# Performance work log

Hardware: AMD Instinct MI355X
Metric: run time of the kernel (lower is better)

Reference implementation:

```python
import jax, jax.numpy as jnp
import numpy as np

QUERY_DIM = 3072
HEADS = 24
HEAD_DIM = 128
INNER = HEADS * HEAD_DIM  # 3072
MLP_HIDDEN = int(QUERY_DIM * 4.0)  # 12288
MLP_MULT = 2
EPS = 1e-5
B, S = 1, 4096


def setup_inputs() -> dict:
    key = jax.random.key(0)
    ks = jax.random.split(key, 8)
    hidden_states = jax.random.normal(ks[0], (B, S, QUERY_DIM), dtype=jnp.float32)
    # rotary angles for half the head dim (interleaved / non-neox style)
    t = jnp.arange(S, dtype=jnp.float32)[:, None]
    inv_freq = 1.0 / (10000.0 ** (jnp.arange(0, HEAD_DIM, 2, dtype=jnp.float32) / HEAD_DIM))
    ang = t * inv_freq[None, :]
    cos = jnp.cos(ang)
    sin = jnp.sin(ang)
    W_qkv_mlp = jax.random.normal(ks[1], (QUERY_DIM, 3 * INNER + MLP_HIDDEN * MLP_MULT), dtype=jnp.float32) * 0.02
    W_out = jax.random.normal(ks[2], (INNER + MLP_HIDDEN, QUERY_DIM), dtype=jnp.float32) * 0.02
    b_out = jnp.zeros((QUERY_DIM,), dtype=jnp.float32)
    norm_q_w = jnp.ones((HEAD_DIM,), dtype=jnp.float32)
    norm_k_w = jnp.ones((HEAD_DIM,), dtype=jnp.float32)
    return {"hidden_states": hidden_states, "cos": cos, "sin": sin,
            "W_qkv_mlp": W_qkv_mlp, "W_out": W_out, "b_out": b_out,
            "norm_q_w": norm_q_w, "norm_k_w": norm_k_w}


def _rmsnorm(x, w, eps=EPS):
    var = jnp.mean(jnp.square(x), axis=-1, keepdims=True)
    return x * jax.lax.rsqrt(var + eps) * w


def _rope_interleaved(x, cos, sin):
    # x: [B,S,H,D]; cos/sin: [S, D//2]. Non-neox: rotate interleaved pairs.
    x1 = x[..., 0::2]
    x2 = x[..., 1::2]
    c = cos[None, :, None, :]
    s = sin[None, :, None, :]
    o1 = x1 * c - x2 * s
    o2 = x2 * c + x1 * s
    return jnp.stack([o1, o2], axis=-1).reshape(x.shape)


def reference(hidden_states, cos, sin, W_qkv_mlp, W_out, b_out, norm_q_w, norm_k_w):
    h = hidden_states @ W_qkv_mlp  # [B,S, 3*INNER + 2*MLP_HIDDEN]
    qkv, mlp = jnp.split(h, [3 * INNER], axis=-1)
    q, k, v = jnp.split(qkv, 3, axis=-1)
    q = q.reshape(B, S, HEADS, HEAD_DIM)
    k = k.reshape(B, S, HEADS, HEAD_DIM)
    v = v.reshape(B, S, HEADS, HEAD_DIM)
    q = _rmsnorm(q, norm_q_w)
    k = _rmsnorm(k, norm_k_w)
    q = _rope_interleaved(q, cos, sin)
    k = _rope_interleaved(k, cos, sin)
    scale = 1.0 / np.sqrt(HEAD_DIM)
    scores = jnp.einsum('bqhd,bkhd->bhqk', q, k) * scale
    probs = jax.nn.softmax(scores, axis=-1)
    attn = jnp.einsum('bhqk,bkhd->bqhd', probs, v)
    attn = attn.reshape(B, S, INNER)
    m1, m2 = jnp.split(mlp, 2, axis=-1)
    mlp_out = jax.nn.silu(m1) * m2
    out = jnp.concatenate([attn, mlp_out], axis=-1) @ W_out + b_out
    return out
```

## Files before the change

### kernel.cpp

```cpp
#include <hip/hip_runtime.h>

typedef short shortx8 __attribute__((ext_vector_type(8)));
typedef short shortx4 __attribute__((ext_vector_type(4)));
typedef float floatx4 __attribute__((ext_vector_type(4)));
typedef float floatx16 __attribute__((ext_vector_type(16)));
typedef unsigned short u16;
typedef unsigned int u32;

#define GLB(x) ((const __attribute__((address_space(1))) void*)(x))
#define LDSC(x) ((__attribute__((address_space(3))) void*)(x))
#define BARRIER()                                  \
  do {                                             \
    __builtin_amdgcn_sched_barrier(0);             \
    __builtin_amdgcn_s_barrier();                  \
    __builtin_amdgcn_sched_barrier(0);             \
  } while (0)
#define WAITV6() asm volatile("s_waitcnt vmcnt(6)" ::: "memory")
#define WAITV8() asm volatile("s_waitcnt vmcnt(8)" ::: "memory")
#define WAITLGKM(N)                                          \
  do {                                                       \
    asm volatile("s_waitcnt lgkmcnt(" #N ")");               \
    __builtin_amdgcn_sched_barrier(0);                       \
  } while (0)

__device__ __forceinline__ float bf2f(u16 u) {
  unsigned x = ((unsigned)u) << 16;
  float f;
  __builtin_memcpy(&f, &x, 4);
  return f;
}
__device__ __forceinline__ u16 f2bf(float f) {
  unsigned x;
  __builtin_memcpy(&x, &f, 4);
  x += 0x7fffu + ((x >> 16) & 1u);
  return (u16)(x >> 16);
}
__device__ __forceinline__ u32 pk_bf16(float lo, float hi) {
  u32 r;
  asm("v_cvt_pk_bf16_f32 %0, %1, %2" : "=v"(r) : "v"(lo), "v"(hi));
  return r;
}

__global__ __launch_bounds__(256) void cast_bf16(const float* __restrict__ src,
                                                 u16* __restrict__ dst) {
  const size_t i = ((size_t)blockIdx.x * 256 + threadIdx.x) << 3;
  floatx4 a = *(const floatx4*)(src + i);
  floatx4 b = *(const floatx4*)(src + i + 4);
  shortx8 o;
#pragma unroll
  for (int e = 0; e < 4; ++e) {
    o[e] = (short)f2bf(a[e]);
    o[e + 4] = (short)f2bf(b[e]);
  }
  *(shortx8*)(dst + i) = o;
}

__global__ __launch_bounds__(256) void transpose_cast(const float* __restrict__ src,
                                                      u16* __restrict__ dst,
                                                      int R, int C, int perm) {
  __shared__ u16 T[64 * 72];
  const int tiles_c = C >> 6;
  const int r0 = (blockIdx.x / tiles_c) << 6;
  const int c0 = (blockIdx.x % tiles_c) << 6;
  const int tid = threadIdx.x;
  const int rl = tid >> 4;
  const int cb = (tid & 15) << 2;
#pragma unroll
  for (int rr = 0; rr < 4; ++rr) {
    const int row = rr * 16 + rl;
    floatx4 v = *(const floatx4*)(src + (size_t)(r0 + row) * C + c0 + cb);
#pragma unroll
    for (int i = 0; i < 4; ++i) T[(cb + i) * 72 + row] = f2bf(v[i]);
  }
  __syncthreads();
  int dbase = c0;
  if (perm && c0 >= 9216) {
    if (c0 < 21504) { const int u = c0 - 9216;  dbase = 9216 + ((u >> 7) << 8) + (u & 64); }
    else            { const int u = c0 - 21504; dbase = 9216 + ((u >> 7) << 8) + 128 + (u & 64); }
  }
#pragma unroll
  for (int ii = 0; ii < 2; ++ii) {
    const int chunk = tid + (ii << 8);
    const int cr = chunk >> 3;
    const int r8 = (chunk & 7) << 3;
    shortx8 v = *(const shortx8*)(T + cr * 72 + r8);
    *(shortx8*)(dst + (size_t)(dbase + cr) * R + r0 + r8) = v;
  }
}

template <int MODE>
__global__ __launch_bounds__(512, 2) void gemm8(const u16* __restrict__ A,
                                                const u16* __restrict__ B,
                                                void* __restrict__ Cout,
                                                u16* __restrict__ CC2,
                                                int M, int N, int K, int Ksub) {
  __shared__ u16 lds[8 * 8192];

  const int nbm = M >> 8;
  const int nwg = nbm * (N >> 8);
  const int cpx = nwg >> 3;
  const int wg = ((int)blockIdx.x & 7) * cpx + ((int)blockIdx.x >> 3);
  const int bm = wg % nbm;
  const int bn = wg / nbm;
  const int koff = (int)blockIdx.y * Ksub;

  const int tid = threadIdx.x;
  const int lane = tid & 63;
  const int w = tid >> 6;
  const int wm = w >> 2;
  const int wn = w & 3;
  const int l15 = lane & 15;
  const int l4 = lane >> 4;
  const int NT = Ksub >> 6;

  const int lrow = lane >> 2;
  const int lblk = lane & 3;

#define UNIT(buf, mat, ks) (lds + (((buf) * 4 + (mat) * 2 + (ks)) << 13))

  const u16* Abase = A + (size_t)bm * 256 * K + koff;
  const u16* Bbase = B + (size_t)bn * 256 * K + koff;

  auto STAGE = [&](int mat, int ks, int buf, int t) {
    const u16* gb = mat ? Bbase : Abase;
#pragma unroll
    for (int j = 0; j < 2; ++j) {
      const int row = (w * 2 + j) * 16 + lrow;
      const int sblk = lblk ^ ((row >> 1) & 3);
      const u16* src = gb + (size_t)row * K + (t << 6) + (ks << 5) + (sblk << 3);
      __builtin_amdgcn_global_load_lds(GLB(src),
                                       LDSC(UNIT(buf, mat, ks) + ((w * 2 + j) << 9)),
                                       16, 0, 0);
    }
  };
  auto LDA = [&](int mf, int ks, int buf) -> shortx8 {
    const int row = wm * 128 + mf * 16 + l15;
    return *(const shortx8*)(UNIT(buf, 0, ks) + row * 32 + ((l4 ^ ((row >> 1) & 3)) << 3));
  };
  auto LDB = [&](int nf, int ks, int buf) -> shortx8 {
    const int row = wn * 64 + nf * 16 + l15;
    return *(const shortx8*)(UNIT(buf, 1, ks) + row * 32 + ((l4 ^ ((row >> 1) & 3)) << 3));
  };

  floatx4 acc[8][4] = {};
  shortx8 a_cur[4], a_nxt[4], b_cur[4], b_nxt[4];

  STAGE(0, 0, 0, 0); STAGE(1, 0, 0, 0);
  STAGE(0, 1, 0, 0); STAGE(1, 1, 0, 0);
  STAGE(0, 0, 1, 1); STAGE(1, 0, 1, 1);
  WAITV8();
  BARRIER();
#pragma unroll
  for (int m = 0; m < 4; ++m) a_cur[m] = LDA(m, 0, 0);
#pragma unroll
  for (int n = 0; n < 4; ++n) b_cur[n] = LDB(n, 0, 0);

#pragma unroll 2
  for (int T = 0; T < NT; ++T) {
    const int cur = T & 1, nxt = cur ^ 1;
    const int t1 = (T + 1 < NT) ? T + 1 : NT - 1;
    const int t2 = (T + 2 < NT) ? T + 2 : NT - 1;

    STAGE(0, 1, nxt, t1);
#pragma unroll
    for (int m = 0; m < 4; ++m) a_nxt[m] = LDA(4 + m, 0, cur);
    WAITLGKM(4);
    __builtin_amdgcn_s_setprio(1);
#pragma unroll
    for (int m = 0; m < 4; ++m)
#pragma unroll
      for (int n = 0; n < 4; ++n)
        acc[m][n] = __builtin_amdgcn_mfma_f32_16x16x32_bf16(a_cur[m], b_cur[n], acc[m][n], 0, 0, 0);
    __builtin_amdgcn_s_setprio(0);
    WAITV6();
    BARRIER();

    STAGE(1, 1, nxt, t1);
#pragma unroll
    for (int m = 0; m < 4; ++m) a_cur[m] = LDA(m, 1, cur);
#pragma unroll
    for (int n = 0; n < 4; ++n) b_nxt[n] = LDB(n, 1, cur);
    WAITLGKM(8);
    __builtin_amdgcn_s_setprio(1);
#pragma unroll
    for (int m = 0; m < 4; ++m)
#pragma unroll
      for (int n = 0; n < 4; ++n)
        acc[4 + m][n] = __builtin_amdgcn_mfma_f32_16x16x32_bf16(a_nxt[m], b_cur[n], acc[4 + m][n], 0, 0, 0);
    __builtin_amdgcn_s_setprio(0);
    BARRIER();

    STAGE(0, 0, cur, t2);
#pragma unroll
    for (int m = 0; m < 4; ++m) a_nxt[m] = LDA(4 + m, 1, cur);
    WAITLGKM(4);
    __builtin_amdgcn_s_setprio(1);
#pragma unroll
    for (int m = 0; m < 4; ++m)
#pragma unroll
      for (int n = 0; n < 4; ++n)
        acc[m][n] = __builtin_amdgcn_mfma_f32_16x16x32_bf16(a_cur[m], b_nxt[n], acc[m][n], 0, 0, 0);
    __builtin_amdgcn_s_setprio(0);
    WAITV6();
    BARRIER();

    STAGE(1, 0, cur, t2);
#pragma unroll
    for (int m = 0; m < 4; ++m) a_cur[m] = LDA(m, 0, nxt);
#pragma unroll
    for (int n = 0; n < 4; ++n) b_cur[n] = LDB(n, 0, nxt);
    WAITLGKM(8);
    __builtin_amdgcn_s_setprio(1);
#pragma unroll
    for (int m = 0; m < 4; ++m)
#pragma unroll
      for (int n = 0; n < 4; ++n)
        acc[4 + m][n] = __builtin_amdgcn_mfma_f32_16x16x32_bf16(a_nxt[m], b_nxt[n], acc[4 + m][n], 0, 0, 0);
    __builtin_amdgcn_s_setprio(0);
    BARRIER();
  }

  const int orow0 = bm * 256 + wm * 128 + (l4 << 2);
  if (MODE == 0) {
    if (bn < 36) {
      u16* C = (u16*)Cout;
      const int ocol0 = bn * 256 + wn * 64 + l15;
#pragma unroll
      for (int m = 0; m < 8; ++m)
#pragma unroll
        for (int n = 0; n < 4; ++n)
#pragma unroll
          for (int r = 0; r < 4; ++r)
            C[(size_t)(orow0 + m * 16 + r) * 9216 + ocol0 + n * 16] = f2bf(acc[m][n][r]);
    } else {
      __syncthreads();
      float* buf = (float*)lds + (wm * 2 + (wn & 1)) * 8192;
      if (wn >= 2) {
#pragma unroll
        for (int m = 0; m < 4; ++m)
#pragma unroll
          for (int n = 0; n < 4; ++n) {
            const int chunk = (m * 4 + l4) ^ (l15 & 7);
            *(floatx4*)(buf + (((n * 16 + l15) << 4) + chunk) * 4) = acc[m][n];
          }
      } else {
#pragma unroll
        for (int m = 0; m < 4; ++m)
#pragma unroll
          for (int n = 0; n < 4; ++n) {
            const int chunk = (m * 4 + l4) ^ (l15 & 7);
            *(floatx4*)(buf + 4096 + (((n * 16 + l15) << 4) + chunk) * 4) = acc[4 + m][n];
          }
      }
      __syncthreads();
      const int gcol0 = 3072 + (bn - 36) * 128 + (wn & 1) * 64 + l15;
      if (wn < 2) {
#pragma unroll
        for (int m = 0; m < 4; ++m)
#pragma unroll
          for (int n = 0; n < 4; ++n) {
            const int chunk = (m * 4 + l4) ^ (l15 & 7);
            const floatx4 m2v = *(const floatx4*)(buf + (((n * 16 + l15) << 4) + chunk) * 4);
#pragma unroll
            for (int r = 0; r < 4; ++r) {
              const float m1 = acc[m][n][r];
              const float sg = 1.0f / (1.0f + exp2f(-1.4426950408889634f * m1));
              CC2[(size_t)(orow0 + m * 16 + r) * 15360 + gcol0 + n * 16] =
                  f2bf(m1 * sg * m2v[r]);
            }
          }
      } else {
#pragma unroll
        for (int m = 0; m < 4; ++m)
#pragma unroll
          for (int n = 0; n < 4; ++n) {
            const int chunk = (m * 4 + l4) ^ (l15 & 7);
            const floatx4 m1v = *(const floatx4*)(buf + 4096 + (((n * 16 + l15) << 4) + chunk) * 4);
#pragma unroll
            for (int r = 0; r < 4; ++r) {
              const float m1 = m1v[r];
              const float sg = 1.0f / (1.0f + exp2f(-1.4426950408889634f * m1));
              CC2[(size_t)(orow0 + (4 + m) * 16 + r) * 15360 + gcol0 + n * 16] =
                  f2bf(m1 * sg * acc[4 + m][n][r]);
            }
          }
      }
    }
  } else {
    float* C = (float*)Cout + (size_t)blockIdx.y * M * N;
    const int ocol0 = bn * 256 + wn * 64 + l15;
#pragma unroll
    for (int m = 0; m < 8; ++m)
#pragma unroll
      for (int n = 0; n < 4; ++n)
#pragma unroll
        for (int r = 0; r < 4; ++r)
          C[(size_t)(orow0 + m * 16 + r) * N + ocol0 + n * 16] = acc[m][n][r];
  }
}
#undef UNIT

__global__ __launch_bounds__(256) void reduce_bias(const float* __restrict__ P,
                                                   const float* __restrict__ bias,
                                                   float* __restrict__ out) {
  const size_t base = ((size_t)blockIdx.x * 256 + threadIdx.x) << 2;
  const size_t stride = (size_t)4096 * 3072;
  floatx4 a = *(const floatx4*)(P + base);
  floatx4 b = *(const floatx4*)(P + stride + base);
  floatx4 c = *(const floatx4*)(P + 2 * stride + base);
  floatx4 d = *(const floatx4*)(P + 3 * stride + base);
  floatx4 bb = *(const floatx4*)(bias + (base % 3072));
  *(floatx4*)(out + base) = a + b + c + d + bb;
}

#define QSCALE (0.08838834764831845f * 1.4426950408889634f)

__global__ __launch_bounds__(256, 2) void qkv_prep(
    const u16* __restrict__ H, const float* __restrict__ cosb,
    const float* __restrict__ sinb, const float* __restrict__ nqw,
    const float* __restrict__ nkw, u16* __restrict__ Qo, u16* __restrict__ Ko,
    u16* __restrict__ Vo) {
  __shared__ u16 VT[128 * 72];
  const int head = blockIdx.y;
  const int t0 = blockIdx.x << 6;
  const int tid = threadIdx.x;
  const int tl = tid >> 2;
  const int db = (tid & 3) << 5;
  const int token = t0 + tl;

  const u16* hp = H + (size_t)token * 9216 + head * 128 + db;
  shortx8 qv[4], kvv[4], vv[4];
#pragma unroll
  for (int i = 0; i < 4; ++i) {
    qv[i] = *(const shortx8*)(hp + i * 8);
    kvv[i] = *(const shortx8*)(hp + 3072 + i * 8);
    vv[i] = *(const shortx8*)(hp + 6144 + i * 8);
  }
  float qx[32], kx[32];
  float sq = 0.f, sk = 0.f;
#pragma unroll
  for (int i = 0; i < 4; ++i)
#pragma unroll
    for (int j = 0; j < 8; ++j) {
      float a = bf2f((u16)qv[i][j]); qx[i * 8 + j] = a; sq += a * a;
      float b = bf2f((u16)kvv[i][j]); kx[i * 8 + j] = b; sk += b * b;
    }
  sq += __shfl_xor(sq, 1); sq += __shfl_xor(sq, 2);
  sk += __shfl_xor(sk, 1); sk += __shfl_xor(sk, 2);
  const float rq = rsqrtf(sq * (1.0f / 128.0f) + 1e-5f);
  const float rk = rsqrtf(sk * (1.0f / 128.0f) + 1e-5f);

  shortx8 oqv[4], okv[4];
#pragma unroll
  for (int p = 0; p < 16; ++p) {
    const float c = cosb[(size_t)token * 64 + (db >> 1) + p];
    const float s = sinb[(size_t)token * 64 + (db >> 1) + p];
    const int vi = p >> 2, vj = (p & 3) << 1;
    float a1 = qx[2 * p] * rq * nqw[db + 2 * p];
    float a2 = qx[2 * p + 1] * rq * nqw[db + 2 * p + 1];
    oqv[vi][vj] = (short)f2bf((a1 * c - a2 * s) * QSCALE);
    oqv[vi][vj + 1] = (short)f2bf((a2 * c + a1 * s) * QSCALE);
    float b1 = kx[2 * p] * rk * nkw[db + 2 * p];
    float b2 = kx[2 * p + 1] * rk * nkw[db + 2 * p + 1];
    okv[vi][vj] = (short)f2bf(b1 * c - b2 * s);
    okv[vi][vj + 1] = (short)f2bf(b2 * c + b1 * s);
  }
  {
    u16* qo = Qo + (size_t)head * 4096 * 128 + (size_t)token * 128 + db;
    u16* ko = Ko + (size_t)head * 4096 * 128 + (size_t)token * 128 + db;
#pragma unroll
    for (int i = 0; i < 4; ++i) {
      *(shortx8*)(qo + i * 8) = oqv[i];
      *(shortx8*)(ko + i * 8) = okv[i];
    }
  }
#pragma unroll
  for (int i = 0; i < 4; ++i)
#pragma unroll
    for (int j = 0; j < 8; ++j) VT[(db + i * 8 + j) * 72 + tl] = (u16)vv[i][j];
  __syncthreads();
#pragma unroll
  for (int ii = 0; ii < 4; ++ii) {
    const int chunk = tid + (ii << 8);
    const int d = chunk >> 3;
    const int j8 = (chunk & 7) << 3;
    shortx8 v = *(const shortx8*)(VT + d * 72 + j8);
    *(shortx8*)(Vo + (size_t)head * 128 * 4096 + (size_t)d * 4096 + t0 + j8) = v;
  }
}

__global__ __launch_bounds__(256, 2) void attn_kernel(const u16* __restrict__ Qg,
                                                      const u16* __restrict__ Kg,
                                                      const u16* __restrict__ Vg,
                                                      u16* __restrict__ CC) {
  __shared__ u16 Ks[128 * 128];
  __shared__ u16 Vs[128 * 128];

  const int head = blockIdx.y;
  const int q0 = blockIdx.x << 7;
  const int tid = threadIdx.x;
  const int lane = tid & 63;
  const int wave = tid >> 6;
  const int l31 = lane & 31;
  const int kh = lane >> 5;

  const u16* Qh = Qg + (size_t)head * 4096 * 128;
  const u16* Kh = Kg + (size_t)head * 4096 * 128;
  const u16* Vh = Vg + (size_t)head * 128 * 4096;

  const int qrow = q0 + wave * 32 + l31;
  shortx8 qf[8];
#pragma unroll
  for (int ks = 0; ks < 8; ++ks)
    qf[ks] = *(const shortx8*)(Qh + (size_t)qrow * 128 + ks * 16 + kh * 8);

  floatx16 ot[4] = {};
  float mrun = -1e30f, lrun = 0.0f;

  for (int s0 = 0; s0 < 4096; s0 += 128) {
#pragma unroll
    for (int i = 0; i < 8; ++i) {
      const int c = wave * 8 + i;
      const int row = c * 4 + (lane >> 4);
      const int blk = (lane & 15) ^ (row & 7);
      __builtin_amdgcn_global_load_lds(GLB(Kh + (size_t)(s0 + row) * 128 + blk * 8),
                                       LDSC(Ks + c * 512), 16, 0, 0);
    }
#pragma unroll
    for (int i = 0; i < 8; ++i) {
      const int c = wave * 8 + i;
      const int row = c * 4 + (lane >> 4);
      const int blk = (lane & 15) ^ (row & 7);
      __builtin_amdgcn_global_load_lds(GLB(Vh + (size_t)row * 4096 + s0 + blk * 8),
                                       LDSC(Vs + c * 512), 16, 0, 0);
    }
    __syncthreads();

    floatx16 st[4] = {};
    __builtin_amdgcn_s_setprio(1);
#pragma unroll
    for (int kvt = 0; kvt < 4; ++kvt) {
      const int krow = kvt * 32 + l31;
#pragma unroll
      for (int ks = 0; ks < 8; ++ks) {
        shortx8 kf = *(const shortx8*)(Ks + krow * 128 + (((ks * 2 + kh) ^ (krow & 7)) << 3));
        st[kvt] = __builtin_amdgcn_mfma_f32_32x32x16_bf16(kf, qf[ks], st[kvt], 0, 0, 0);
      }
    }
    __builtin_amdgcn_s_setprio(0);

    float vmax = st[0][0];
#pragma unroll
    for (int t = 0; t < 4; ++t)
#pragma unroll
      for (int r = 0; r < 16; ++r) vmax = fmaxf(vmax, st[t][r]);
    vmax = fmaxf(vmax, __shfl_xor(vmax, 32));
    const float mn = fmaxf(mrun, vmax);
    const float alpha = exp2f(mrun - mn);
    mrun = mn;

    float rs = 0.0f;
#pragma unroll
    for (int t = 0; t < 4; ++t)
#pragma unroll
      for (int r = 0; r < 16; ++r) {
        const float p = exp2f(st[t][r] - mn);
        st[t][r] = p;
        rs += p;
      }
    rs += __shfl_xor(rs, 32);
    lrun = lrun * alpha + rs;
    if (__any(alpha < 1.0f)) {
#pragma unroll
      for (int dt = 0; dt < 4; ++dt)
#pragma unroll
        for (int r = 0; r < 16; ++r) ot[dt][r] *= alpha;
    }

    u32 w[4][8];
#pragma unroll
    for (int t = 0; t < 4; ++t)
#pragma unroll
      for (int q = 0; q < 4; ++q) {
        w[t][2 * q] = pk_bf16(st[t][4 * q], st[t][4 * q + 1]);
        w[t][2 * q + 1] = pk_bf16(st[t][4 * q + 2], st[t][4 * q + 3]);
      }

#pragma unroll
    for (int ks = 0; ks < 8; ++ks) {
      const int kvt = ks >> 1;
      const int qA = 2 * (ks & 1);
      const u32 wA0 = w[kvt][2 * qA], wA1 = w[kvt][2 * qA + 1];
      const u32 wB0 = w[kvt][2 * qA + 2], wB1 = w[kvt][2 * qA + 3];
      const u32 send0 = kh ? wA0 : wB0;
      const u32 send1 = kh ? wA1 : wB1;
      const u32 r0 = (u32)__shfl_xor((int)send0, 32);
      const u32 r1 = (u32)__shfl_xor((int)send1, 32);
      u32 fw[4];
      fw[0] = kh ? r0 : wA0;
      fw[1] = kh ? r1 : wA1;
      fw[2] = kh ? wB0 : r0;
      fw[3] = kh ? wB1 : r1;
      shortx8 pf;
      __builtin_memcpy(&pf, fw, 16);
      __builtin_amdgcn_s_setprio(1);
#pragma unroll
      for (int dt = 0; dt < 4; ++dt) {
        const int vrow = dt * 32 + l31;
        shortx8 vf = *(const shortx8*)(Vs + vrow * 128 + (((ks * 2 + kh) ^ (vrow & 7)) << 3));
        ot[dt] = __builtin_amdgcn_mfma_f32_32x32x16_bf16(vf, pf, ot[dt], 0, 0, 0);
      }
      __builtin_amdgcn_s_setprio(0);
    }
    __syncthreads();
  }

  const float inv = 1.0f / lrun;
  u16* outp = CC + (size_t)qrow * 15360 + head * 128;
#pragma unroll
  for (int dt = 0; dt < 4; ++dt)
#pragma unroll
    for (int g = 0; g < 4; ++g) {
      shortx4 pack;
#pragma unroll
      for (int r = 0; r < 4; ++r) pack[r] = (short)f2bf(ot[dt][4 * g + r] * inv);
      *(shortx4*)(outp + dt * 32 + g * 8 + kh * 4) = pack;
    }
}

extern "C" void kernel_launch(void* const* d_in, const int* in_sizes, int n_in,
                              void* d_out, int out_size, void* d_ws, size_t ws_size,
                              hipStream_t stream) {
  const float* hs = (const float*)d_in[0];
  const float* cosb = (const float*)d_in[1];
  const float* sinb = (const float*)d_in[2];
  const float* w1 = (const float*)d_in[3];
  const float* wout = (const float*)d_in[4];
  const float* bout = (const float*)d_in[5];
  const float* nqw = (const float*)d_in[6];
  const float* nkw = (const float*)d_in[7];
  float* out = (float*)d_out;

  char* ws = (char*)d_ws;
  u16* X16 = (u16*)ws; ws += (size_t)4096 * 3072 * 2;
  u16* W1T = (u16*)ws; ws += (size_t)33792 * 3072 * 2;
  u16* WOT = (u16*)ws; ws += (size_t)3072 * 15360 * 2;
  u16* H   = (u16*)ws; ws += (size_t)4096 * 33792 * 2;
  u16* Qb  = (u16*)ws; ws += (size_t)24 * 4096 * 128 * 2;
  u16* Kb  = (u16*)ws; ws += (size_t)24 * 4096 * 128 * 2;
  u16* VTb = (u16*)ws; ws += (size_t)24 * 4096 * 128 * 2;
  u16* CC  = (u16*)ws; ws += (size_t)4096 * 15360 * 2;
  float* Pk = (float*)H;

  cast_bf16<<<6144, 256, 0, stream>>>(hs, X16);
  transpose_cast<<<(3072 / 64) * (33792 / 64), 256, 0, stream>>>(w1, W1T, 3072, 33792, 1);
  transpose_cast<<<(15360 / 64) * (3072 / 64), 256, 0, stream>>>(wout, WOT, 15360, 3072, 0);
  gemm8<0><<<(4096 / 256) * (33792 / 256), 512, 0, stream>>>(X16, W1T, H, CC,
                                                             4096, 33792, 3072, 3072);
  qkv_prep<<<dim3(64, 24), 256, 0, stream>>>(H, cosb, sinb, nqw, nkw, Qb, Kb, VTb);
  attn_kernel<<<dim3(32, 24), 256, 0, stream>>>(Qb, Kb, VTb, CC);
  gemm8<1><<<dim3((4096 / 256) * (3072 / 256), 4), 512, 0, stream>>>(
      CC, WOT, Pk, nullptr, 4096, 3072, 15360, 3840);
  reduce_bias<<<(4096 * 3072 / 4) / 256, 256, 0, stream>>>(Pk, bout, out);
}
```

Baseline: 1.746 ms.

## Write transposed V directly from QKV GEMM epilogue and remap attention blocks

The first GEMM's epilogue now writes the V columns straight into the per-head transposed V buffer, so V no longer goes through H. qkv_prep therefore drops its V load and LDS transpose. Attention blocks are launched on a 1D grid with an XCD-aware swizzle so that blocks of the same head land on the same chiplet, which should improve K/V cache reuse. The V epilogue stores are strided 8-byte writes along tokens, which may coalesce less well than the previous row-major stores.

```diff
diff --git a/kernel.cpp b/kernel.cpp
--- a/kernel.cpp
+++ b/kernel.cpp
@@ -93,6 +93,7 @@
                                                 const u16* __restrict__ B,
                                                 void* __restrict__ Cout,
                                                 u16* __restrict__ CC2,
+                                                u16* __restrict__ VTb,
                                                 int M, int N, int K, int Ksub) {
   __shared__ u16 lds[8 * 8192];
 
@@ -222,7 +223,7 @@
 
   const int orow0 = bm * 256 + wm * 128 + (l4 << 2);
   if (MODE == 0) {
-    if (bn < 36) {
+    if (bn < 24) {
       u16* C = (u16*)Cout;
       const int ocol0 = bn * 256 + wn * 64 + l15;
 #pragma unroll
@@ -232,6 +233,21 @@
 #pragma unroll
           for (int r = 0; r < 4; ++r)
             C[(size_t)(orow0 + m * 16 + r) * 9216 + ocol0 + n * 16] = f2bf(acc[m][n][r]);
+    } else if (bn < 36) {
+      const int hbase = (bn - 24) * 2 + (wn >> 1);
+      const int dbase = (wn & 1) * 64 + l15;
+      u16* vt = VTb + (size_t)hbase * 524288;
+#pragma unroll
+      for (int m = 0; m < 8; ++m) {
+        const int tq = bm * 256 + wm * 128 + m * 16 + (l4 << 2);
+#pragma unroll
+        for (int n = 0; n < 4; ++n) {
+          shortx4 pk;
+#pragma unroll
+          for (int r = 0; r < 4; ++r) pk[r] = (short)f2bf(acc[m][n][r]);
+          *(shortx4*)(vt + (size_t)(dbase + n * 16) * 4096 + tq) = pk;
+        }
+      }
     } else {
       __syncthreads();
       float* buf = (float*)lds + (wm * 2 + (wn & 1)) * 8192;
@@ -318,9 +334,7 @@
 __global__ __launch_bounds__(256, 2) void qkv_prep(
     const u16* __restrict__ H, const float* __restrict__ cosb,
     const float* __restrict__ sinb, const float* __restrict__ nqw,
-    const float* __restrict__ nkw, u16* __restrict__ Qo, u16* __restrict__ Ko,
-    u16* __restrict__ Vo) {
-  __shared__ u16 VT[128 * 72];
+    const float* __restrict__ nkw, u16* __restrict__ Qo, u16* __restrict__ Ko) {
   const int head = blockIdx.y;
   const int t0 = blockIdx.x << 6;
   const int tid = threadIdx.x;
@@ -329,12 +343,11 @@
   const int token = t0 + tl;
 
   const u16* hp = H + (size_t)token * 9216 + head * 128 + db;
-  shortx8 qv[4], kvv[4], vv[4];
+  shortx8 qv[4], kvv[4];
 #pragma unroll
   for (int i = 0; i < 4; ++i) {
     qv[i] = *(const shortx8*)(hp + i * 8);
     kvv[i] = *(const shortx8*)(hp + 3072 + i * 8);
-    vv[i] = *(const shortx8*)(hp + 6144 + i * 8);
   }
   float qx[32], kx[32];
   float sq = 0.f, sk = 0.f;
@@ -365,27 +378,12 @@
     okv[vi][vj] = (short)f2bf(b1 * c - b2 * s);
     okv[vi][vj + 1] = (short)f2bf(b2 * c + b1 * s);
   }
-  {
-    u16* qo = Qo + (size_t)head * 4096 * 128 + (size_t)token * 128 + db;
-    u16* ko = Ko + (size_t)head * 4096 * 128 + (size_t)token * 128 + db;
-#pragma unroll
-    for (int i = 0; i < 4; ++i) {
-      *(shortx8*)(qo + i * 8) = oqv[i];
-      *(shortx8*)(ko + i * 8) = okv[i];
-    }
-  }
-#pragma unroll
-  for (int i = 0; i < 4; ++i)
-#pragma unroll
-    for (int j = 0; j < 8; ++j) VT[(db + i * 8 + j) * 72 + tl] = (u16)vv[i][j];
-  __syncthreads();
-#pragma unroll
-  for (int ii = 0; ii < 4; ++ii) {
-    const int chunk = tid + (ii << 8);
-    const int d = chunk >> 3;
-    const int j8 = (chunk & 7) << 3;
-    shortx8 v = *(const shortx8*)(VT + d * 72 + j8);
-    *(shortx8*)(Vo + (size_t)head * 128 * 4096 + (size_t)d * 4096 + t0 + j8) = v;
+  u16* qo = Qo + (size_t)head * 4096 * 128 + (size_t)token * 128 + db;
+  u16* ko = Ko + (size_t)head * 4096 * 128 + (size_t)token * 128 + db;
+#pragma unroll
+  for (int i = 0; i < 4; ++i) {
+    *(shortx8*)(qo + i * 8) = oqv[i];
+    *(shortx8*)(ko + i * 8) = okv[i];
   }
 }
 
@@ -396,8 +394,10 @@
   __shared__ u16 Ks[128 * 128];
   __shared__ u16 Vs[128 * 128];
 
-  const int head = blockIdx.y;
-  const int q0 = blockIdx.x << 7;
+  const int bid = (int)blockIdx.x;
+  const int sid = (bid & 7) * 96 + (bid >> 3);
+  const int head = sid >> 5;
+  const int q0 = (sid & 31) << 7;
   const int tid = threadIdx.x;
   const int lane = tid & 63;
   const int wave = tid >> 6;
@@ -555,11 +555,11 @@
   cast_bf16<<<6144, 256, 0, stream>>>(hs, X16);
   transpose_cast<<<(3072 / 64) * (33792 / 64), 256, 0, stream>>>(w1, W1T, 3072, 33792, 1);
   transpose_cast<<<(15360 / 64) * (3072 / 64), 256, 0, stream>>>(wout, WOT, 15360, 3072, 0);
-  gemm8<0><<<(4096 / 256) * (33792 / 256), 512, 0, stream>>>(X16, W1T, H, CC,
+  gemm8<0><<<(4096 / 256) * (33792 / 256), 512, 0, stream>>>(X16, W1T, H, CC, VTb,
                                                              4096, 33792, 3072, 3072);
-  qkv_prep<<<dim3(64, 24), 256, 0, stream>>>(H, cosb, sinb, nqw, nkw, Qb, Kb, VTb);
-  attn_kernel<<<dim3(32, 24), 256, 0, stream>>>(Qb, Kb, VTb, CC);
+  qkv_prep<<<dim3(64, 24), 256, 0, stream>>>(H, cosb, sinb, nqw, nkw, Qb, Kb);
+  attn_kernel<<<768, 256, 0, stream>>>(Qb, Kb, VTb, CC);
   gemm8<1><<<dim3((4096 / 256) * (3072 / 256), 4), 512, 0, stream>>>(
-      CC, WOT, Pk, nullptr, 4096, 3072, 15360, 3840);
+      CC, WOT, Pk, nullptr, nullptr, 4096, 3072, 15360, 3840);
   reduce_bias<<<(4096 * 3072 / 4) / 256, 256, 0, stream>>>(Pk, bout, out);
 }
```

Result: no change. 1.753 ms (median of 3 runs) (+0.4%).
